# Kernel tuning notes

Measured on AMD Instinct MI355X. Metric: run time of the kernel, lower is better.

Reference implementation:

```python
import jax, jax.numpy as jnp
import numpy as np

WIN = (6, 6, 6)
HEADS = 4
DIM = 96
SPATIAL = (48, 48, 48)


def _window_partition(x, ws):
    # x: (b, d, h, w, c) -> (num_windows*b, wd*wh*ww, c)
    b, d, h, w, c = x.shape
    wd, wh, ww = ws
    x = x.reshape(b, d // wd, wd, h // wh, wh, w // ww, ww, c)
    x = x.transpose(0, 1, 3, 5, 2, 4, 6, 7)
    return x.reshape(-1, wd * wh * ww, c)


def _window_reverse(win, ws, b, d, h, w, c):
    wd, wh, ww = ws
    x = win.reshape(b, d // wd, h // wh, w // ww, wd, wh, ww, c)
    x = x.transpose(0, 1, 4, 2, 5, 3, 6, 7)
    return x.reshape(b, d, h, w, c)


def _rel_index(ws):
    # static numpy computation of relative-position index table, (n, n) int
    wd, wh, ww = ws
    coords = np.stack(np.meshgrid(np.arange(wd), np.arange(wh), np.arange(ww), indexing='ij'))
    cf = coords.reshape(3, -1)
    rc = (cf[:, :, None] - cf[:, None, :]).transpose(1, 2, 0).astype(np.int64)
    rc[..., 0] += wd - 1
    rc[..., 1] += wh - 1
    rc[..., 2] += ww - 1
    rc[..., 0] *= (2 * wh - 1) * (2 * ww - 1)
    rc[..., 1] *= (2 * ww - 1)
    return rc.sum(-1)


def _shift_mask(d, h, w, ws, ss):
    # static numpy mask, (nW, n, n) float32 with 0 / -100
    wd, wh, ww = ws
    sd, sh, sw = ss
    m = np.zeros((1, d, h, w, 1), np.float32)
    cnt = 0
    for dsl in (slice(0, -wd), slice(-wd, -sd), slice(-sd, None)):
        for hsl in (slice(0, -wh), slice(-wh, -sh), slice(-sh, None)):
            for wsl in (slice(0, -ww), slice(-ww, -sw), slice(-sw, None)):
                m[:, dsl, hsl, wsl, :] = cnt
                cnt += 1
    mw = m.reshape(1, d // wd, wd, h // wh, wh, w // ww, ww, 1)
    mw = mw.transpose(0, 1, 3, 5, 2, 4, 6, 7).reshape(-1, wd * wh * ww)
    am = mw[:, None, :] - mw[:, :, None]
    return np.where(am != 0, np.float32(-100.0), np.float32(0.0))


def _conv1x1(x, W, b):
    # 1x1x1 Conv3d == channel matmul; x: (b,c,d,h,w), W: (out,in)
    return jnp.einsum('bcdhw,oc->bodhw', x, W) + b[None, :, None, None, None]


def setup_inputs() -> dict:
    key = jax.random.key(0)
    ks = jax.random.split(key, 12)
    shp = (1, DIM) + SPATIAL
    table_size = (2 * WIN[0] - 1) * (2 * WIN[1] - 1) * (2 * WIN[2] - 1)
    s = 1.0 / np.sqrt(DIM)
    return {
        'q_in': jax.random.normal(ks[0], shp, jnp.float32),
        'k_in': jax.random.normal(ks[1], shp, jnp.float32),
        'v_in': jax.random.normal(ks[2], shp, jnp.float32),
        'Wq': jax.random.normal(ks[3], (DIM, DIM), jnp.float32) * s,
        'bq': jnp.zeros((DIM,), jnp.float32),
        'Wk': jax.random.normal(ks[4], (DIM, DIM), jnp.float32) * s,
        'bk': jnp.zeros((DIM,), jnp.float32),
        'Wv': jax.random.normal(ks[5], (DIM, DIM), jnp.float32) * s,
        'bv': jnp.zeros((DIM,), jnp.float32),
        'Wp': jax.random.normal(ks[6], (DIM, DIM), jnp.float32) * s,
        'bp': jnp.zeros((DIM,), jnp.float32),
        'rel_table': jax.random.normal(ks[7], (table_size, HEADS), jnp.float32) * 0.02,
        'use_shift': 1,
    }


def reference(q_in, k_in, v_in, Wq, bq, Wk, bk, Wv, bv, Wp, bp, rel_table, use_shift):
    b, c, d, h, w = q_in.shape
    wd, wh, ww = WIN
    hd = DIM // HEADS
    scale = hd ** -0.5
    shift = bool(use_shift)
    ss = (wd // 2, wh // 2, ww // 2) if shift else (0, 0, 0)

    q = _conv1x1(q_in, Wq, bq)
    k = _conv1x1(k_in, Wk, bk)
    v = _conv1x1(v_in, Wv, bv)
    # d,h,w divisible by window -> no padding needed
    if shift:
        q = jnp.roll(q, (-ss[0], -ss[1], -ss[2]), axis=(2, 3, 4))
        k = jnp.roll(k, (-ss[0], -ss[1], -ss[2]), axis=(2, 3, 4))
        v = jnp.roll(v, (-ss[0], -ss[1], -ss[2]), axis=(2, 3, 4))

    qw = _window_partition(q.transpose(0, 2, 3, 4, 1), WIN)
    kw = _window_partition(k.transpose(0, 2, 3, 4, 1), WIN)
    vw = _window_partition(v.transpose(0, 2, 3, 4, 1), WIN)
    nw, n, _ = qw.shape
    qw = qw.reshape(nw, n, HEADS, hd).transpose(0, 2, 1, 3)
    kw = kw.reshape(nw, n, HEADS, hd).transpose(0, 2, 1, 3)
    vw = vw.reshape(nw, n, HEADS, hd).transpose(0, 2, 1, 3)

    attn = jnp.einsum('whnd,whmd->whnm', qw * scale, kw)  # (nw, H, n, n)
    idx = _rel_index(WIN)
    bias = rel_table[idx.reshape(-1)].reshape(n, n, HEADS).transpose(2, 0, 1)
    attn = attn + bias[None]
    if shift:
        mask = jnp.asarray(_shift_mask(d, h, w, WIN, ss))  # (nW, n, n)
        nW = mask.shape[0]
        attn = attn.reshape(b, nW, HEADS, n, n) + mask[None, :, None]
        attn = attn.reshape(nw, HEADS, n, n)
    attn = jax.nn.softmax(attn, axis=-1)
    out = jnp.einsum('whnm,whmd->whnd', attn, vw)
    out = out.transpose(0, 2, 1, 3).reshape(nw, n, c)
    out = _window_reverse(out, WIN, b, d, h, w, c)
    if shift:
        out = jnp.roll(out, ss, axis=(1, 2, 3))
    out = out.transpose(0, 4, 1, 2, 3)
    out = _conv1x1(out, Wp, bp)
    return out
```

## Files before the change

### kernel.cpp

```cpp
#include <hip/hip_runtime.h>
#include <hip/hip_bf16.h>


#define CH    96
#define DS    48
#define NVOX  (48*48*48)
#define WSZ   6
#define NWIN  512
#define NTOK  216
#define NTOKP 224
#define NHEADS 4
#define HD    24
#define XSTR  100
#define VSTR  228
#define PGRID (NVOX / 128)
#define CEXP  8.0f

typedef __attribute__((ext_vector_type(4))) float  f32x4;
typedef __attribute__((ext_vector_type(4))) short  s16x4;
typedef __attribute__((ext_vector_type(8))) short  s16x8;
typedef __attribute__((ext_vector_type(8))) _Float16 f16x8;

static __device__ inline short f2b(float f) {
    union { float f; unsigned u; } v; v.f = f;
    unsigned r = v.u + 0x7FFF + ((v.u >> 16) & 1);
    return (short)(r >> 16);
}
static __device__ inline float bf2f(short s) {
    union { unsigned u; float f; } v;
    v.u = ((unsigned)(unsigned short)s) << 16;
    return v.f;
}
static __device__ inline unsigned pack_f16(float a, float b) {
    unsigned short ua = __builtin_bit_cast(unsigned short, (_Float16)a);
    unsigned short ub = __builtin_bit_cast(unsigned short, (_Float16)b);
    return (unsigned)ua | ((unsigned)ub << 16);
}

__global__ __launch_bounds__(256) void proj_mfma_kernel(
    const float* __restrict__ x0, const float* __restrict__ x1, const float* __restrict__ x2,
    const float* __restrict__ W0, const float* __restrict__ W1, const float* __restrict__ W2,
    const float* __restrict__ b0, const float* __restrict__ b1, const float* __restrict__ b2,
    const int* __restrict__ use_shift,
    short* __restrict__ d0, short* __restrict__ d1, short* __restrict__ d2,
    float scale0)
{
    __shared__ short Xs[128 * XSTR];
    __shared__ short Wb[CH * XSTR];

    int tid = threadIdx.x;
    int which = blockIdx.x / PGRID;
    int bx = blockIdx.x - which * PGRID;
    int v0 = bx * 128;

    const float* x    = (which == 0) ? x0 : ((which == 1) ? x1 : x2);
    const float* W    = (which == 0) ? W0 : ((which == 1) ? W1 : W2);
    const float* bias = (which == 0) ? b0 : ((which == 1) ? b1 : b2);
    short*       dst  = (which == 0) ? d0 : ((which == 1) ? d1 : d2);
    float scale = (which == 0) ? scale0 : 1.0f;

    for (int e = tid; e < CH * 48; e += 256) {
        int oc = e / 48, kp = e - oc * 48;
        float2 wv = *(const float2*)&W[oc * CH + 2 * kp];
        *(unsigned*)&Wb[oc * XSTR + 2 * kp] = pack_f16(wv.x, wv.y);
    }
    {
        int vox = tid & 127;
        int v = v0 + vox;
        int d = v / (DS * DS);
        int rem = v - d * DS * DS;
        int h = rem / DS;
        int w = rem - h * DS;
        int s = (use_shift[0] != 0) ? 3 : 0;
        int sd = d + s; if (sd >= DS) sd -= DS;
        int s_h = h + s; if (s_h >= DS) s_h -= DS;
        int s_w = w + s; if (s_w >= DS) s_w -= DS;
        int src = (sd * DS + s_h) * DS + s_w;
        for (int e = tid; e < 128 * 48; e += 256) {
            int kp = e >> 7;
            float xa = x[(2 * kp) * NVOX + src];
            float xb = x[(2 * kp + 1) * NVOX + src];
            *(unsigned*)&Xs[vox * XSTR + 2 * kp] = pack_f16(xa, xb);
        }
    }
    __syncthreads();

    const int wid = tid >> 6;
    const int lane = tid & 63;
    const int g = lane >> 4;
    const int c = lane & 15;
    const int mrow = wid * 32;

    const f32x4 zero4 = {0.f, 0.f, 0.f, 0.f};
    f32x4 acc[2][6];
#pragma unroll
    for (int i = 0; i < 2; i++)
#pragma unroll
        for (int j = 0; j < 6; j++) acc[i][j] = zero4;

#pragma unroll
    for (int kt = 0; kt < 3; kt++) {
        const short* pa0 = &Xs[(mrow + c) * XSTR + kt * 32 + g * 8];
        s16x4 a0l = *(const s16x4*)pa0;
        s16x4 a0h = *(const s16x4*)(pa0 + 4);
        f16x8 a0 = __builtin_bit_cast(f16x8,
            __builtin_shufflevector(a0l, a0h, 0, 1, 2, 3, 4, 5, 6, 7));
        const short* pa1 = &Xs[(mrow + 16 + c) * XSTR + kt * 32 + g * 8];
        s16x4 a1l = *(const s16x4*)pa1;
        s16x4 a1h = *(const s16x4*)(pa1 + 4);
        f16x8 a1 = __builtin_bit_cast(f16x8,
            __builtin_shufflevector(a1l, a1h, 0, 1, 2, 3, 4, 5, 6, 7));
#pragma unroll
        for (int nt = 0; nt < 6; nt++) {
            const short* pb = &Wb[(nt * 16 + c) * XSTR + kt * 32 + g * 8];
            s16x4 bl = *(const s16x4*)pb;
            s16x4 bh = *(const s16x4*)(pb + 4);
            f16x8 bb = __builtin_bit_cast(f16x8,
                __builtin_shufflevector(bl, bh, 0, 1, 2, 3, 4, 5, 6, 7));
            acc[0][nt] = __builtin_amdgcn_mfma_f32_16x16x32_f16(a0, bb, acc[0][nt], 0, 0, 0);
            acc[1][nt] = __builtin_amdgcn_mfma_f32_16x16x32_f16(a1, bb, acc[1][nt], 0, 0, 0);
        }
    }

    float bs[6];
#pragma unroll
    for (int nt = 0; nt < 6; nt++) bs[nt] = bias[nt * 16 + c];

    __syncthreads();

#pragma unroll
    for (int mtile = 0; mtile < 2; mtile++)
#pragma unroll
        for (int nt = 0; nt < 6; nt++)
#pragma unroll
            for (int r = 0; r < 4; r++) {
                int vox = mrow + mtile * 16 + g * 4 + r;
                int oc = nt * 16 + c;
                Xs[vox * XSTR + oc] = f2b((acc[mtile][nt][r] + bs[nt]) * scale);
            }
    __syncthreads();

    for (int e = tid; e < 512; e += 256) {
        int vox = e >> 2, q = e & 3;
        int v = v0 + vox;
        int d = v / (DS * DS);
        int rem = v - d * DS * DS;
        int h = rem / DS;
        int w = rem - h * DS;
        int widx = (d / WSZ) * 64 + (h / WSZ) * 8 + (w / WSZ);
        int tok  = (d % WSZ) * 36 + (h % WSZ) * WSZ + (w % WSZ);
        short* dp = dst + ((size_t)(widx * NHEADS + q) * NTOK + tok) * HD;
        const short* sp = &Xs[vox * XSTR + q * 24];
        s16x4 a0 = *(const s16x4*)(sp);
        s16x4 a1 = *(const s16x4*)(sp + 4);
        s16x4 a2 = *(const s16x4*)(sp + 8);
        s16x4 a3 = *(const s16x4*)(sp + 12);
        s16x4 a4 = *(const s16x4*)(sp + 16);
        s16x4 a5 = *(const s16x4*)(sp + 20);
        *(s16x8*)(dp)      = __builtin_shufflevector(a0, a1, 0, 1, 2, 3, 4, 5, 6, 7);
        *(s16x8*)(dp + 8)  = __builtin_shufflevector(a2, a3, 0, 1, 2, 3, 4, 5, 6, 7);
        *(s16x8*)(dp + 16) = __builtin_shufflevector(a4, a5, 0, 1, 2, 3, 4, 5, 6, 7);
    }
}

__global__ __launch_bounds__(256) void attn_mfma_kernel(
    const short* __restrict__ qw, const short* __restrict__ kw,
    const short* __restrict__ vw, const float* __restrict__ rel_table,
    const int* __restrict__ use_shift, short* __restrict__ aw)
{
    __shared__ short Ks[NTOK * 36];
    __shared__ short Vt[32 * VSTR];
    __shared__ short PO[4][576];
    __shared__ short eg_s[NTOKP];
    __shared__ float Lb[1331];

    int widx = blockIdx.x >> 2;
    int head = blockIdx.x & 3;
    int tid = threadIdx.x;
    bool shift = (use_shift[0] != 0);
    int wd = widx >> 6, wh = (widx >> 3) & 7, ww = widx & 7;

    {
        int* z2 = (int*)Ks; int* z3 = (int*)Vt;
        for (int i = tid; i < NTOK * 18; i += 256) z2[i] = 0;
        for (int i = tid; i < 16 * VSTR; i += 256) z3[i] = 0;
    }
    for (int i = tid; i < 1331; i += 256) Lb[i] = rel_table[i * NHEADS + head];
    __syncthreads();

    const size_t hbase = (size_t)(widx * NHEADS + head) * NTOK * HD;

    for (int e = tid; e < NTOK * 3; e += 256) {
        int t = e / 3, ch = e - t * 3;
        const short* kp = kw + hbase + t * 24 + ch * 8;
        s16x8 k8 = *(const s16x8*)kp;
        *(s16x4*)&Ks[t * 36 + ch * 8]     = __builtin_shufflevector(k8, k8, 0, 1, 2, 3);
        *(s16x4*)&Ks[t * 36 + ch * 8 + 4] = __builtin_shufflevector(k8, k8, 4, 5, 6, 7);
        s16x8 v8 = *(const s16x8*)(vw + hbase + t * 24 + ch * 8);
#pragma unroll
        for (int j = 0; j < 8; j++) Vt[(ch * 8 + j) * VSTR + t] = v8[j];
    }
    for (int t = tid; t < NTOKP; t += 256) {
        int e = 0, g = 0;
        if (t < NTOK) {
            int td = t / 36, th = (t / 6) % 6, tw = t % 6;
            e = td * 121 + th * 11 + tw;
            if (shift) {
                int cd = wd * 6 + td, chh = wh * 6 + th, cw = ww * 6 + tw;
                int gd = (cd < 42) ? 0 : ((cd < 45) ? 1 : 2);
                int gh = (chh < 42) ? 0 : ((chh < 45) ? 1 : 2);
                int gw = (cw < 42) ? 0 : ((cw < 45) ? 1 : 2);
                g = gd * 9 + gh * 3 + gw;
            }
        }
        eg_s[t] = (short)(e | (g << 10));
    }
    __syncthreads();

    const int wid = tid >> 6;
    const int lane = tid & 63;
    const int g = lane >> 4;
    const int c = lane & 15;

    const f32x4 zero4 = {0.f, 0.f, 0.f, 0.f};
    short* myPs = &PO[wid][0];

    for (int mt = wid; mt < 14; mt += 4) {
        int m0 = mt * 16;
        s16x8 aq = {0, 0, 0, 0, 0, 0, 0, 0};
        int qtok = m0 + c;
        if (g < 3 && qtok < NTOK)
            aq = *(const s16x8*)(qw + hbase + (size_t)qtok * HD + g * 8);
        f32x4 sreg[14];
#pragma unroll
        for (int t = 0; t < 14; t++) {
            int krow = (t < 13) ? (t * 16 + c) : (208 + (c & 7));
            const short* p = &Ks[krow * 36 + g * 8];
            s16x4 lo = *(const s16x4*)p;
            s16x4 hi = *(const s16x4*)(p + 4);
            s16x8 bk = __builtin_shufflevector(lo, hi, 0, 1, 2, 3, 4, 5, 6, 7);
            sreg[t] = __builtin_amdgcn_mfma_f32_16x16x32_bf16(aq, bk, zero4, 0, 0, 0);
        }
        int gi[4], ei[4];
#pragma unroll
        for (int r = 0; r < 4; r++) {
            int eg = eg_s[m0 + g * 4 + r];
            ei[r] = eg & 1023;
            gi[r] = eg >> 10;
        }
        float sm[4] = {0.f, 0.f, 0.f, 0.f};
#pragma unroll
        for (int t = 0; t < 13; t++) {
            int j = t * 16 + c;
            int eg = eg_s[j];
            int ej = eg & 1023, gj = eg >> 10;
#pragma unroll
            for (int r = 0; r < 4; r++) {
                float s = sreg[t][r] + Lb[ei[r] - ej + 665];
                if (gi[r] != gj) s -= 100.f;
                float e = __expf(s - CEXP);
                sreg[t][r] = e;
                sm[r] += e;
            }
        }
        {
            int j = 208 + c;
            int eg = eg_s[j];
            int ej = eg & 1023, gj = eg >> 10;
            bool padc = (c >= 8);
#pragma unroll
            for (int r = 0; r < 4; r++) {
                float s = sreg[13][r] + Lb[ei[r] - ej + 665];
                if (gi[r] != gj) s -= 100.f;
                float e = padc ? 0.f : __expf(s - CEXP);
                sreg[13][r] = e;
                sm[r] += e;
            }
        }
#pragma unroll
        for (int o = 1; o < 16; o <<= 1)
#pragma unroll
            for (int r = 0; r < 4; r++) sm[r] += __shfl_xor(sm[r], o);
        float rinv[4];
#pragma unroll
        for (int r = 0; r < 4; r++) rinv[r] = 1.f / sm[r];

        f32x4 o0 = zero4, o1 = zero4;
#pragma unroll
        for (int kt = 0; kt < 7; kt++) {
#pragma unroll
            for (int tt = 0; tt < 2; tt++) {
                int t = kt * 2 + tt;
#pragma unroll
                for (int r = 0; r < 4; r++)
                    myPs[(g * 4 + r) * 36 + tt * 16 + c] = f2b(sreg[t][r]);
            }
            const short* p = &myPs[c * 36 + g * 8];
            s16x4 lo = *(const s16x4*)p;
            s16x4 hi = *(const s16x4*)(p + 4);
            s16x8 ap = __builtin_shufflevector(lo, hi, 0, 1, 2, 3, 4, 5, 6, 7);
            const short* pv0 = &Vt[c * VSTR + kt * 32 + g * 8];
            s16x4 v0l = *(const s16x4*)pv0;
            s16x4 v0h = *(const s16x4*)(pv0 + 4);
            s16x8 bv0 = __builtin_shufflevector(v0l, v0h, 0, 1, 2, 3, 4, 5, 6, 7);
            const short* pv1 = &Vt[(16 + c) * VSTR + kt * 32 + g * 8];
            s16x4 v1l = *(const s16x4*)pv1;
            s16x4 v1h = *(const s16x4*)(pv1 + 4);
            s16x8 bv1 = __builtin_shufflevector(v1l, v1h, 0, 1, 2, 3, 4, 5, 6, 7);
            o0 = __builtin_amdgcn_mfma_f32_16x16x32_bf16(ap, bv0, o0, 0, 0, 0);
            o1 = __builtin_amdgcn_mfma_f32_16x16x32_bf16(ap, bv1, o1, 0, 0, 0);
        }

#pragma unroll
        for (int r = 0; r < 4; r++) {
            int row = g * 4 + r;
            myPs[row * 24 + c] = f2b(o0[r] * rinv[r]);
            if (c < 8) myPs[row * 24 + 16 + c] = f2b(o1[r] * rinv[r]);
        }
        int nrow = NTOK - m0; if (nrow > 16) nrow = 16;
        int nsh = nrow * 24;
        short* dstw = aw + hbase + (size_t)m0 * HD;
        for (int j = lane; j * 8 < nsh; j += 64)
            *(s16x8*)(dstw + j * 8) = *(const s16x8*)(myPs + j * 8);
    }
}

__global__ __launch_bounds__(256) void out_proj_mfma_kernel(
    const short* __restrict__ aw, const float* __restrict__ Wp,
    const float* __restrict__ bp, const int* __restrict__ use_shift,
    float* __restrict__ out)
{
    __shared__ short Xs[128 * XSTR];
    __shared__ short Wb[CH * XSTR];

    int tid = threadIdx.x;
    int v0 = blockIdx.x * 128;

    for (int e = tid; e < CH * 48; e += 256) {
        int oc = e / 48, kp = e - oc * 48;
        float2 wv = *(const float2*)&Wp[oc * CH + 2 * kp];
        *(unsigned*)&Wb[oc * XSTR + 2 * kp] = pack_f16(wv.x, wv.y);
    }
    for (int e = tid; e < 512; e += 256) {
        int vox = e >> 2, hq = e & 3;
        int v = v0 + vox;
        int d = v / (DS * DS);
        int rem = v - d * DS * DS;
        int h = rem / DS;
        int w = rem - h * DS;
        int s = (use_shift[0] != 0) ? 3 : 0;
        int sd = d - s; if (sd < 0) sd += DS;
        int s_h = h - s; if (s_h < 0) s_h += DS;
        int s_w = w - s; if (s_w < 0) s_w += DS;
        int widx = (sd / WSZ) * 64 + (s_h / WSZ) * 8 + (s_w / WSZ);
        int tok  = (sd % WSZ) * 36 + (s_h % WSZ) * WSZ + (s_w % WSZ);
        const short* sp = aw + ((size_t)(widx * NHEADS + hq) * NTOK + tok) * HD;
#pragma unroll
        for (int j3 = 0; j3 < 3; j3++) {
            s16x8 a = *(const s16x8*)(sp + 8 * j3);
#pragma unroll
            for (int p = 0; p < 4; p++)
                *(unsigned*)&Xs[vox * XSTR + hq * 24 + 8 * j3 + 2 * p] =
                    pack_f16(bf2f(a[2 * p]), bf2f(a[2 * p + 1]));
        }
    }
    __syncthreads();

    const int wid = tid >> 6;
    const int lane = tid & 63;
    const int g = lane >> 4;
    const int c = lane & 15;

    const f32x4 zero4 = {0.f, 0.f, 0.f, 0.f};
    f32x4 acc[2][6];
#pragma unroll
    for (int i = 0; i < 2; i++)
#pragma unroll
        for (int j = 0; j < 6; j++) acc[i][j] = zero4;

#pragma unroll
    for (int kt = 0; kt < 3; kt++) {
        f16x8 bfr[2];
#pragma unroll
        for (int mi = 0; mi < 2; mi++) {
            const short* pb = &Xs[((2 * wid + mi) * 16 + c) * XSTR + kt * 32 + g * 8];
            s16x4 bl = *(const s16x4*)pb;
            s16x4 bh = *(const s16x4*)(pb + 4);
            bfr[mi] = __builtin_bit_cast(f16x8,
                __builtin_shufflevector(bl, bh, 0, 1, 2, 3, 4, 5, 6, 7));
        }
#pragma unroll
        for (int nt = 0; nt < 6; nt++) {
            const short* pa = &Wb[(nt * 16 + c) * XSTR + kt * 32 + g * 8];
            s16x4 al = *(const s16x4*)pa;
            s16x4 ah = *(const s16x4*)(pa + 4);
            f16x8 af = __builtin_bit_cast(f16x8,
                __builtin_shufflevector(al, ah, 0, 1, 2, 3, 4, 5, 6, 7));
            acc[0][nt] = __builtin_amdgcn_mfma_f32_16x16x32_f16(af, bfr[0], acc[0][nt], 0, 0, 0);
            acc[1][nt] = __builtin_amdgcn_mfma_f32_16x16x32_f16(af, bfr[1], acc[1][nt], 0, 0, 0);
        }
    }

#pragma unroll
    for (int nt = 0; nt < 6; nt++)
#pragma unroll
        for (int r = 0; r < 4; r++) {
            int oc = nt * 16 + g * 4 + r;
            float bb = bp[oc];
#pragma unroll
            for (int mi = 0; mi < 2; mi++) {
                int vox = v0 + (2 * wid + mi) * 16 + c;
                out[(size_t)oc * NVOX + vox] = acc[mi][nt][r] + bb;
            }
        }
}

extern "C" void kernel_launch(void* const* d_in, const int* in_sizes, int n_in,
                              void* d_out, int out_size, void* d_ws, size_t ws_size,
                              hipStream_t stream)
{
    const float* q_in = (const float*)d_in[0];
    const float* k_in = (const float*)d_in[1];
    const float* v_in = (const float*)d_in[2];
    const float* Wq   = (const float*)d_in[3];
    const float* bq   = (const float*)d_in[4];
    const float* Wk   = (const float*)d_in[5];
    const float* bk   = (const float*)d_in[6];
    const float* Wv   = (const float*)d_in[7];
    const float* bv   = (const float*)d_in[8];
    const float* Wp   = (const float*)d_in[9];
    const float* bp   = (const float*)d_in[10];
    const float* rel_table = (const float*)d_in[11];
    const int*   use_shift = (const int*)d_in[12];

    const size_t NELEM = (size_t)NWIN * NTOK * CH;
    short* qw = (short*)d_ws;
    short* kw = qw + NELEM;
    short* vw = kw + NELEM;
    short* aw = vw + NELEM;

    const float scale = 0.20412414523193154f;

    proj_mfma_kernel<<<3 * PGRID, 256, 0, stream>>>(
        q_in, k_in, v_in, Wq, Wk, Wv, bq, bk, bv, use_shift, qw, kw, vw, scale);
    attn_mfma_kernel<<<NWIN * NHEADS, 256, 0, stream>>>(qw, kw, vw, rel_table, use_shift, aw);
    out_proj_mfma_kernel<<<PGRID, 256, 0, stream>>>(aw, Wp, bp, use_shift, (float*)d_out);
}
```

Before: 304.2 us.

## Precompute exp(bias+mask) tables and fold softmax row-sum into PV MMA

Adds a prologue kernel that builds, per head and per shift-window type (8 boundary classes), a padded 224x224 table of exp(rel_bias - C) with masked entries set to zero. The attention kernel then computes exp(score) times the table value, instead of doing the bias lookup, mask compare and shifted exp per element. The row sum is obtained by putting a column of ones into the padded V^T rows, so the second MFMA produces it directly and the shuffle reductions disappear. The cost is an extra kernel writing about 6.4 MB, global-memory reads of that table in the hot loop, and dropping the constant subtraction inside exp, which risks overflow for large scores.

```diff
diff --git a/kernel.cpp b/kernel.cpp
--- a/kernel.cpp
+++ b/kernel.cpp
@@ -35,6 +35,30 @@
     unsigned short ua = __builtin_bit_cast(unsigned short, (_Float16)a);
     unsigned short ub = __builtin_bit_cast(unsigned short, (_Float16)b);
     return (unsigned)ua | ((unsigned)ub << 16);
+}
+
+__global__ __launch_bounds__(256) void eb_kernel(
+    const float* __restrict__ rel_table, float* __restrict__ EB)
+{
+    int idx = blockIdx.x * 256 + threadIdx.x;
+    int head = idx / (8 * NTOKP * NTOKP);
+    int rem = idx - head * 8 * NTOKP * NTOKP;
+    int ty = rem / (NTOKP * NTOKP);
+    int rem2 = rem - ty * NTOKP * NTOKP;
+    int i = rem2 / NTOKP;
+    int j = rem2 - (rem2 / NTOKP) * NTOKP;
+    float val = 0.f;
+    if (i < NTOK && j < NTOK) {
+        int tdi = i / 36, thi = (i / 6) % 6, twi = i % 6;
+        int tdj = j / 36, thj = (j / 6) % 6, twj = j % 6;
+        bool m = ((ty & 1) && ((tdi < 3) != (tdj < 3))) ||
+                 ((ty & 2) && ((thi < 3) != (thj < 3))) ||
+                 ((ty & 4) && ((twi < 3) != (twj < 3)));
+        int ridx = ((tdi - tdj + 5) * 11 + (thi - thj + 5)) * 11 + (twi - twj + 5);
+        float b = rel_table[ridx * NHEADS + head];
+        val = m ? 0.f : __expf(b - CEXP);
+    }
+    EB[idx] = val;
 }
 
 __global__ __launch_bounds__(256) void proj_mfma_kernel(
@@ -165,27 +189,26 @@
 
 __global__ __launch_bounds__(256) void attn_mfma_kernel(
     const short* __restrict__ qw, const short* __restrict__ kw,
-    const short* __restrict__ vw, const float* __restrict__ rel_table,
+    const short* __restrict__ vw, const float* __restrict__ EB,
     const int* __restrict__ use_shift, short* __restrict__ aw)
 {
     __shared__ short Ks[NTOK * 36];
     __shared__ short Vt[32 * VSTR];
     __shared__ short PO[4][576];
-    __shared__ short eg_s[NTOKP];
-    __shared__ float Lb[1331];
 
     int widx = blockIdx.x >> 2;
     int head = blockIdx.x & 3;
     int tid = threadIdx.x;
     bool shift = (use_shift[0] != 0);
     int wd = widx >> 6, wh = (widx >> 3) & 7, ww = widx & 7;
+    int ty = shift ? ((wd == 7 ? 1 : 0) | (wh == 7 ? 2 : 0) | (ww == 7 ? 4 : 0)) : 0;
 
     {
         int* z2 = (int*)Ks; int* z3 = (int*)Vt;
         for (int i = tid; i < NTOK * 18; i += 256) z2[i] = 0;
-        for (int i = tid; i < 16 * VSTR; i += 256) z3[i] = 0;
-    }
-    for (int i = tid; i < 1331; i += 256) Lb[i] = rel_table[i * NHEADS + head];
+        for (int i = tid; i < 16 * VSTR; i += 256)
+            z3[i] = (i >= 12 * VSTR && i < (25 * VSTR) / 2) ? 0x3F803F80 : 0;
+    }
     __syncthreads();
 
     const size_t hbase = (size_t)(widx * NHEADS + head) * NTOK * HD;
@@ -200,21 +223,6 @@
 #pragma unroll
         for (int j = 0; j < 8; j++) Vt[(ch * 8 + j) * VSTR + t] = v8[j];
     }
-    for (int t = tid; t < NTOKP; t += 256) {
-        int e = 0, g = 0;
-        if (t < NTOK) {
-            int td = t / 36, th = (t / 6) % 6, tw = t % 6;
-            e = td * 121 + th * 11 + tw;
-            if (shift) {
-                int cd = wd * 6 + td, chh = wh * 6 + th, cw = ww * 6 + tw;
-                int gd = (cd < 42) ? 0 : ((cd < 45) ? 1 : 2);
-                int gh = (chh < 42) ? 0 : ((chh < 45) ? 1 : 2);
-                int gw = (cw < 42) ? 0 : ((cw < 45) ? 1 : 2);
-                g = gd * 9 + gh * 3 + gw;
-            }
-        }
-        eg_s[t] = (short)(e | (g << 10));
-    }
     __syncthreads();
 
     const int wid = tid >> 6;
@@ -224,6 +232,7 @@
 
     const f32x4 zero4 = {0.f, 0.f, 0.f, 0.f};
     short* myPs = &PO[wid][0];
+    const float* EBt = EB + (size_t)(head * 8 + ty) * NTOKP * NTOKP;
 
     for (int mt = wid; mt < 14; mt += 4) {
         int m0 = mt * 16;
@@ -241,49 +250,15 @@
             s16x8 bk = __builtin_shufflevector(lo, hi, 0, 1, 2, 3, 4, 5, 6, 7);
             sreg[t] = __builtin_amdgcn_mfma_f32_16x16x32_bf16(aq, bk, zero4, 0, 0, 0);
         }
-        int gi[4], ei[4];
-#pragma unroll
-        for (int r = 0; r < 4; r++) {
-            int eg = eg_s[m0 + g * 4 + r];
-            ei[r] = eg & 1023;
-            gi[r] = eg >> 10;
-        }
-        float sm[4] = {0.f, 0.f, 0.f, 0.f};
-#pragma unroll
-        for (int t = 0; t < 13; t++) {
-            int j = t * 16 + c;
-            int eg = eg_s[j];
-            int ej = eg & 1023, gj = eg >> 10;
-#pragma unroll
-            for (int r = 0; r < 4; r++) {
-                float s = sreg[t][r] + Lb[ei[r] - ej + 665];
-                if (gi[r] != gj) s -= 100.f;
-                float e = __expf(s - CEXP);
-                sreg[t][r] = e;
-                sm[r] += e;
-            }
-        }
-        {
-            int j = 208 + c;
-            int eg = eg_s[j];
-            int ej = eg & 1023, gj = eg >> 10;
-            bool padc = (c >= 8);
-#pragma unroll
-            for (int r = 0; r < 4; r++) {
-                float s = sreg[13][r] + Lb[ei[r] - ej + 665];
-                if (gi[r] != gj) s -= 100.f;
-                float e = padc ? 0.f : __expf(s - CEXP);
-                sreg[13][r] = e;
-                sm[r] += e;
-            }
-        }
-#pragma unroll
-        for (int o = 1; o < 16; o <<= 1)
-#pragma unroll
-            for (int r = 0; r < 4; r++) sm[r] += __shfl_xor(sm[r], o);
-        float rinv[4];
-#pragma unroll
-        for (int r = 0; r < 4; r++) rinv[r] = 1.f / sm[r];
+        const float* ebr[4];
+#pragma unroll
+        for (int r = 0; r < 4; r++)
+            ebr[r] = EBt + (size_t)(m0 + g * 4 + r) * NTOKP + c;
+#pragma unroll
+        for (int t = 0; t < 14; t++)
+#pragma unroll
+            for (int r = 0; r < 4; r++)
+                sreg[t][r] = __expf(sreg[t][r]) * ebr[r][t * 16];
 
         f32x4 o0 = zero4, o1 = zero4;
 #pragma unroll
@@ -313,9 +288,11 @@
 
 #pragma unroll
         for (int r = 0; r < 4; r++) {
+            float sm = __shfl(o1[r], (lane & 48) + 8);
+            float ri = 1.f / sm;
             int row = g * 4 + r;
-            myPs[row * 24 + c] = f2b(o0[r] * rinv[r]);
-            if (c < 8) myPs[row * 24 + 16 + c] = f2b(o1[r] * rinv[r]);
+            myPs[row * 24 + c] = f2b(o0[r] * ri);
+            if (c < 8) myPs[row * 24 + 16 + c] = f2b(o1[r] * ri);
         }
         int nrow = NTOK - m0; if (nrow > 16) nrow = 16;
         int nsh = nrow * 24;
@@ -438,11 +415,13 @@
     short* kw = qw + NELEM;
     short* vw = kw + NELEM;
     short* aw = vw + NELEM;
+    float* EB = (float*)(aw + NELEM);
 
     const float scale = 0.20412414523193154f;
 
+    eb_kernel<<<NHEADS * 8 * NTOKP * NTOKP / 256, 256, 0, stream>>>(rel_table, EB);
     proj_mfma_kernel<<<3 * PGRID, 256, 0, stream>>>(
         q_in, k_in, v_in, Wq, Wk, Wv, bq, bk, bv, use_shift, qw, kw, vw, scale);
-    attn_mfma_kernel<<<NWIN * NHEADS, 256, 0, stream>>>(qw, kw, vw, rel_table, use_shift, aw);
+    attn_mfma_kernel<<<NWIN * NHEADS, 256, 0, stream>>>(qw, kw, vw, EB, use_shift, aw);
     out_proj_mfma_kernel<<<PGRID, 256, 0, stream>>>(aw, Wp, bp, use_shift, (float*)d_out);
 }
```

Measured after the change: 279.0 us. -8.3%, faster.
